# Optimization experiments

Measured on AMD Instinct MI355X. Metric: run time of the kernel, lower is better.

## Reference

```python
import jax, jax.numpy as jnp
import numpy as np

C_S, C_Z, C_H, H, PQ, PV = 384, 128, 16, 12, 4, 8
B, N = 1, 512
W_C = (2.0 / (9.0 * PQ)) ** 0.5
W_L = (1.0 / 3.0) ** 0.5
OUT_IN = H * C_Z + H * C_H + H * PV * 3 + H * PV  # 2112


def setup_inputs() -> dict:
    key = jax.random.key(0)
    ks = jax.random.split(key, 16)
    s_i = jax.random.normal(ks[0], (B, N, C_S), jnp.float32)
    z_ij = jax.random.normal(ks[1], (B, N, N, C_Z), jnp.float32)
    # random rotation matrices via QR
    raw = jax.random.normal(ks[2], (B, N, 3, 3), jnp.float32)
    q, r = jnp.linalg.qr(raw)
    rots = q * jnp.sign(jnp.diagonal(r, axis1=-2, axis2=-1))[..., None, :]
    trans = jax.random.normal(ks[3], (B, N, 3), jnp.float32)
    sc = lambda fan_in: 1.0 / np.sqrt(fan_in)
    Wq = jax.random.normal(ks[4], (C_S, H * C_H), jnp.float32) * sc(C_S)
    Wk = jax.random.normal(ks[5], (C_S, H * C_H), jnp.float32) * sc(C_S)
    Wv = jax.random.normal(ks[6], (C_S, H * C_H), jnp.float32) * sc(C_S)
    Wqp = jax.random.normal(ks[7], (C_S, H * PQ * 3), jnp.float32) * sc(C_S)
    Wkp = jax.random.normal(ks[8], (C_S, H * PQ * 3), jnp.float32) * sc(C_S)
    Wvp = jax.random.normal(ks[9], (C_S, H * PV * 3), jnp.float32) * sc(C_S)
    Wb = jax.random.normal(ks[10], (C_Z, H), jnp.float32) * sc(C_Z)
    gamma = jax.random.normal(ks[11], (1, 1, 1, H), jnp.float32)
    Wout = jax.random.normal(ks[12], (OUT_IN, C_S), jnp.float32) * sc(OUT_IN)
    bout = jnp.zeros((C_S,), jnp.float32)
    return dict(s_i=s_i, z_ij=z_ij, rots=rots, trans=trans, Wq=Wq, Wk=Wk, Wv=Wv,
                Wqp=Wqp, Wkp=Wkp, Wvp=Wvp, Wb=Wb, gamma=gamma, Wout=Wout, bout=bout)


def reference(s_i, z_ij, rots, trans, Wq, Wk, Wv, Wqp, Wkp, Wvp, Wb, gamma, Wout, bout):
    b, n = s_i.shape[0], s_i.shape[1]
    q_h = (s_i @ Wq).reshape(b, n, H, C_H)
    k_h = (s_i @ Wk).reshape(b, n, H, C_H)
    v_h = (s_i @ Wv).reshape(b, n, H, C_H)
    q_hp = (s_i @ Wqp).reshape(b, n, H, PQ, 3)
    k_hp = (s_i @ Wkp).reshape(b, n, H, PQ, 3)
    v_hp = (s_i @ Wvp).reshape(b, n, H, PV, 3)
    b_ij = z_ij @ Wb  # (b,i,j,h)

    t = trans[:, :, None, None, :]  # (b,i,1,1,3)
    apply = lambda x: jnp.einsum('bixy,bihpy->bihpx', rots, x) + t
    inv_apply = lambda x: jnp.einsum('bixy,bihpx->bihpy', rots, x - t)

    qg = apply(q_hp)  # (b,i,h,p,3) global frame
    kg = apply(k_hp)
    # pairwise rigid point distance term: (b,i,j,h)
    diff = qg[:, :, None] - kg[:, None]  # (b,i,j,h,p,3)
    dist2 = jnp.sum(diff * diff, axis=(-1, -2))

    a_s = jnp.einsum('bihd,bjhd->bijh', q_h, k_h) / (C_H ** 0.5)
    a_rigid = (W_C / 2.0) * gamma * dist2
    a = jax.nn.softmax(W_L * (a_s + b_ij - a_rigid), axis=-2)  # softmax over j

    o_hat = jnp.einsum('bijh,bijd->bihd', a, z_ij)
    o = jnp.einsum('bijh,bjhd->bihd', a, v_h)
    vg = apply(v_hp)  # (b,j,h,p,3)
    o_hp = inv_apply(jnp.einsum('bijh,bjhpx->bihpx', a, vg))  # (b,i,h,pv,3)
    o_hp_norm = jnp.sqrt(jnp.sum(o_hp * o_hp, axis=-1))  # (b,i,h,pv)

    cat = jnp.concatenate([
        o_hat.reshape(b, n, H * C_Z),
        o.reshape(b, n, H * C_H),
        o_hp.reshape(b, n, H * PV * 3),
        o_hp_norm.reshape(b, n, H * PV),
    ], axis=-1)
    return cat @ Wout + bout
```

## Files before the change

### kernel.cpp

```cpp
#include <hip/hip_runtime.h>
#include <hip/hip_bf16.h>
#include <math.h>

#define NRES 512
#define CS   384
#define CZ   128
#define NH   12
#define PW   1152
#define JB   64
#define NCH  8
#define PSTRIDE32 1040
#define KS   6
#define KAW  352

static constexpr float WL_F      = 0.57735026918962576f;
static constexpr float HALF_WC_F = 0.11785113019775792f;

typedef __attribute__((ext_vector_type(8))) short short8v;
typedef __attribute__((ext_vector_type(4))) float floatx4;

__device__ __forceinline__ ushort f2b(float f) {
    union { float f; uint u; } v; v.f = f;
    return (ushort)((v.u + 0x7FFFu + ((v.u >> 16) & 1u)) >> 16);
}
__device__ __forceinline__ float b2f(ushort b) {
    union { uint u; float f; } v; v.u = ((uint)b) << 16; return v.f;
}

__global__ __launch_bounds__(256) void k_prep(
    const float* __restrict__ Wq, const float* __restrict__ Wk,
    const float* __restrict__ Wv, const float* __restrict__ Wqp,
    const float* __restrict__ Wkp, const float* __restrict__ Wvp,
    const float* __restrict__ Wb, const float* __restrict__ Wout,
    float* __restrict__ Wcat, ushort* __restrict__ wbt16,
    ushort* __restrict__ woT)
{
    __shared__ ushort tile[64][72];
    const int bx = blockIdx.x;
    if (bx < 384) {
        const int c = bx;
        for (int col = threadIdx.x; col < PW; col += 256) {
            float v;
            if (col < 192)      v = Wq [(size_t)c * 192 + col];
            else if (col < 384) v = Wk [(size_t)c * 192 + col - 192];
            else if (col < 576) v = Wv [(size_t)c * 192 + col - 384];
            else if (col < 720) v = Wqp[(size_t)c * 144 + col - 576];
            else if (col < 864) v = Wkp[(size_t)c * 144 + col - 720];
            else                v = Wvp[(size_t)c * 288 + col - 864];
            Wcat[(size_t)c * PW + col] = v;
        }
        if (bx == 0) {
            for (int idx = threadIdx.x; idx < 16 * 128; idx += 256) {
                const int h = idx >> 7, cc = idx & 127;
                wbt16[idx] = (h < NH) ? f2b(WL_F * Wb[(size_t)cc * NH + h]) : (ushort)0;
            }
        }
    } else {
        const int t = bx - 384;
        const int k0 = (t % 33) * 64, c0 = (t / 33) * 64;
        for (int idx = threadIdx.x; idx < 4096; idx += 256) {
            const int r = idx >> 6, c = idx & 63;
            tile[r][c] = f2b(Wout[(size_t)(k0 + r) * 384 + c0 + c]);
        }
        __syncthreads();
        for (int idx = threadIdx.x; idx < 4096; idx += 256) {
            const int c = idx >> 6, r = idx & 63;
            woT[(size_t)(c0 + c) * 2112 + k0 + r] = tile[r][c];
        }
    }
}

__global__ __launch_bounds__(256) void k_gemm(
    const float* __restrict__ s, const float* __restrict__ Wcat,
    const float* __restrict__ rots, const float* __restrict__ trans,
    float* __restrict__ P)
{
    const int tid = threadIdx.x;
    const int tx = tid & 15, ty = tid >> 4;
    const int n0 = blockIdx.x * 48;
    const int m0 = blockIdx.y * 32;
    __shared__ float As[32][34];
    __shared__ float Bs[32][50];
    __shared__ float rot_lds[32][12];

    if (n0 >= 576) {
        for (int idx = tid; idx < 32 * 12; idx += 256) {
            int r = idx / 12, q = idx % 12;
            rot_lds[r][q] = (q < 9) ? rots[(size_t)(m0 + r) * 9 + q]
                                    : trans[(size_t)(m0 + r) * 3 + q - 9];
        }
    }

    float acc[2][3];
    #pragma unroll
    for (int u = 0; u < 2; ++u)
        #pragma unroll
        for (int v = 0; v < 3; ++v) acc[u][v] = 0.f;

    for (int k0 = 0; k0 < CS; k0 += 32) {
        __syncthreads();
        #pragma unroll
        for (int l = 0; l < 4; ++l) {
            int idx = tid + l * 256;
            int kk = idx & 31, r = idx >> 5;
            As[kk][r] = s[(size_t)(m0 + r) * CS + k0 + kk];
        }
        #pragma unroll
        for (int l = 0; l < 6; ++l) {
            int idx = tid + l * 256;
            int kk = idx / 48, cc = idx % 48;
            Bs[kk][cc] = Wcat[(size_t)(k0 + kk) * PW + n0 + cc];
        }
        __syncthreads();
        #pragma unroll
        for (int kk = 0; kk < 32; ++kk) {
            const float2 a = *(const float2*)&As[kk][ty * 2];
            const float b0 = Bs[kk][tx * 3], b1 = Bs[kk][tx * 3 + 1], b2 = Bs[kk][tx * 3 + 2];
            acc[0][0] += a.x * b0; acc[0][1] += a.x * b1; acc[0][2] += a.x * b2;
            acc[1][0] += a.y * b0; acc[1][1] += a.y * b1; acc[1][2] += a.y * b2;
        }
    }

    #pragma unroll
    for (int u = 0; u < 2; ++u) {
        float v0 = acc[u][0], v1 = acc[u][1], v2 = acc[u][2];
        if (n0 >= 576) {
            const float* RT = rot_lds[ty * 2 + u];
            const float p0 = v0, p1 = v1, p2 = v2;
            v0 = RT[0] * p0 + RT[1] * p1 + RT[2] * p2 + RT[9];
            v1 = RT[3] * p0 + RT[4] * p1 + RT[5] * p2 + RT[10];
            v2 = RT[6] * p0 + RT[7] * p1 + RT[8] * p2 + RT[11];
        }
        float* dst = P + (size_t)(m0 + ty * 2 + u) * PW + n0 + tx * 3;
        dst[0] = v0; dst[1] = v1; dst[2] = v2;
    }
}

__global__ __launch_bounds__(128) void k_ka(
    const float* __restrict__ P, ushort* __restrict__ Kfull,
    ushort* __restrict__ vp2)
{
    const int j = blockIdx.x;
    const int tid = threadIdx.x;
    __shared__ float njs[NH];
    const float* prow = P + (size_t)j * PW;
    const float* kr  = prow + 192;
    const float* vr  = prow + 384;
    const float* kgr = prow + 720;
    const float* vgr = prow + 864;
    if (tid < NH) {
        float s = 0.f;
        #pragma unroll
        for (int e = 0; e < 12; ++e) { const float v = kgr[tid * 12 + e]; s += v * v; }
        njs[tid] = s;
    }
    __syncthreads();
    ushort* dst = Kfull + (size_t)j * KAW;
    for (int t = tid; t < KAW; t += 128) {
        float v;
        if (t < 192)       v = kr[t];
        else if (t < 336)  v = kgr[t - 192];
        else if (t < 348)  v = njs[t - 336];
        else if (t == 348) v = 1.0f;
        else               v = 0.f;
        dst[t] = f2b(v);
    }
    const int p = j >> 1, par = j & 1;
    for (int c = tid; c < 480; c += 128) {
        const float v = (c < 192) ? vr[c] : vgr[c - 192];
        vp2[((size_t)p * 480 + c) * 2 + par] = f2b(v);
    }
}

__global__ __launch_bounds__(256, 6) void k_flash(
    const float* __restrict__ z, const ushort* __restrict__ wbt16,
    const float* __restrict__ gamma, const float* __restrict__ P,
    const ushort* __restrict__ Kfull, const ushort* __restrict__ vp2,
    uint* __restrict__ part)
{
    const int i   = blockIdx.x;
    const int jc  = blockIdx.y;
    const int j0  = jc * JB;
    const int tid = threadIdx.x;
    const int wid = tid >> 6, lane = tid & 63;

    __shared__ __align__(16) short zbT[128 * JB];
    __shared__ __align__(16) char  uni[10240];
    __shared__ float pm[NH], ps[NH];

    short*  BfT     = (short*)uni;
    float*  ltf     = (float*)uni;
    short*  ltb     = (short*)(uni + 4352);
    float4* halfacc = (float4*)(uni + 6400);

    uint* pb32   = part + ((size_t)i * NCH + jc) * PSTRIDE32;
    ushort* pb16 = (ushort*)pb32;
    float* pbf   = (float*)pb32;

    const int jb = wid * 16 + (lane & 15);
    const int ko = (lane >> 4) * 8;

    short8v af[4];
    {
        const float* za = z + ((size_t)i * NRES + j0 + jb) * CZ + ko;
        #pragma unroll
        for (int m = 0; m < 4; ++m) {
            const float4 f0 = *(const float4*)(za + m * 32);
            const float4 f1 = *(const float4*)(za + m * 32 + 4);
            short8v a;
            a[0] = (short)f2b(f0.x); a[1] = (short)f2b(f0.y);
            a[2] = (short)f2b(f0.z); a[3] = (short)f2b(f0.w);
            a[4] = (short)f2b(f1.x); a[5] = (short)f2b(f1.y);
            a[6] = (short)f2b(f1.z); a[7] = (short)f2b(f1.w);
            af[m] = a;
            #pragma unroll
            for (int e = 0; e < 8; ++e) {
                const int c = ko + m * 32 + e;
                zbT[c * 64 + (((jb >> 3) ^ (c & 7)) * 8) + (jb & 7)] = a[e];
            }
        }
    }
    {
        const float* prow = P + (size_t)i * PW;
        for (int t = tid; t < 12 * 352; t += 256) {
            const int h = t / 352, k = t - h * 352;
            float v = 0.f;
            if (k < 192) {
                if ((k >> 4) == h) v = 0.25f * WL_F * prow[k];
            } else if (k < 336) {
                const int e = k - 192;
                if (e / 12 == h) v = 2.f * HALF_WC_F * WL_F * gamma[h] * prow[576 + e];
            } else if (k < 348) {
                if (k - 336 == h) v = -HALF_WC_F * WL_F * gamma[h];
            } else if (k == 348) {
                float ss = 0.f;
                #pragma unroll
                for (int e = 0; e < 12; ++e) {
                    const float x = prow[576 + h * 12 + e];
                    ss += x * x;
                }
                v = -HALF_WC_F * WL_F * gamma[h] * ss;
            }
            BfT[t] = (short)f2b(v);
        }
    }
    __syncthreads();

    floatx4 lacc = {0.f, 0.f, 0.f, 0.f};
    {
        const int n  = lane & 15;
        const int nb = (n < NH) ? n : 0;
        const ushort* arow = Kfull + (size_t)(j0 + jb) * KAW + ko;
        const short*  brow = &BfT[nb * 352 + ko];
        const ushort* wrow = wbt16 + n * 128 + ko;
        #pragma unroll
        for (int st = 0; st < 11; ++st) {
            const short8v a = *(const short8v*)(arow + st * 32);
            const short8v b = *(const short8v*)(brow + st * 32);
            lacc = __builtin_amdgcn_mfma_f32_16x16x32_bf16(a, b, lacc, 0, 0, 0);
        }
        #pragma unroll
        for (int st = 0; st < 4; ++st) {
            const short8v b = *(const short8v*)(wrow + st * 32);
            lacc = __builtin_amdgcn_mfma_f32_16x16x32_bf16(af[st], b, lacc, 0, 0, 0);
        }
    }
    __syncthreads();
    {
        const int n = lane & 15;
        #pragma unroll
        for (int r = 0; r < 4; ++r)
            ltf[n * 68 + wid * 16 + (lane >> 4) * 4 + r] = lacc[r];
    }
    __syncthreads();

    if (tid < 192) {
        const int h = tid >> 4, s = tid & 15;
        float4 v = *(const float4*)&ltf[h * 68 + s * 4];
        float m = fmaxf(fmaxf(v.x, v.y), fmaxf(v.z, v.w));
        #pragma unroll
        for (int o = 1; o < 16; o <<= 1) m = fmaxf(m, __shfl_xor(m, o));
        float4 e;
        e.x = __expf(v.x - m); e.y = __expf(v.y - m);
        e.z = __expf(v.z - m); e.w = __expf(v.w - m);
        float sum = e.x + e.y + e.z + e.w;
        #pragma unroll
        for (int o = 1; o < 16; o <<= 1) sum += __shfl_xor(sum, o);
        *(float4*)&ltf[h * 68 + s * 4] = e;
        const uint lo = (uint)f2b(e.x) | ((uint)f2b(e.y) << 16);
        const uint hi = (uint)f2b(e.z) | ((uint)f2b(e.w) << 16);
        uint* dst = (uint*)&ltb[h * 64 + (((s >> 1) ^ (h & 7)) * 8) + (s & 1) * 4];
        dst[0] = lo; dst[1] = hi;
        if (s == 0) { pm[h] = m; ps[h] = sum; }
    } else {
        const int tt = tid - 192;
        uint* dst = (uint*)&ltb[(12 + (tt >> 4)) * 64 + (tt & 15) * 4];
        dst[0] = 0u; dst[1] = 0u;
    }
    __syncthreads();

    {
        const int hrow = lane & 15;
        const int u0 = (lane >> 4), u1 = u0 + 4;
        const short8v a0 = *(const short8v*)&ltb[hrow * 64 + ((u0 ^ (hrow & 7)) * 8)];
        const short8v a1 = *(const short8v*)&ltb[hrow * 64 + ((u1 ^ (hrow & 7)) * 8)];
        #pragma unroll
        for (int t = 0; t < 2; ++t) {
            const int d = (wid * 2 + t) * 16 + (lane & 15);
            const short8v b0 = *(const short8v*)&zbT[d * 64 + ((u0 ^ (d & 7)) * 8)];
            const short8v b1 = *(const short8v*)&zbT[d * 64 + ((u1 ^ (d & 7)) * 8)];
            floatx4 acc = {0.f, 0.f, 0.f, 0.f};
            acc = __builtin_amdgcn_mfma_f32_16x16x32_bf16(a0, b0, acc, 0, 0, 0);
            acc = __builtin_amdgcn_mfma_f32_16x16x32_bf16(a1, b1, acc, 0, 0, 0);
            #pragma unroll
            for (int r = 0; r < 4; ++r) {
                const int h = u0 * 4 + r;
                if (h < NH) pb16[h * 128 + d] = f2b(acc[r]);
            }
        }
    }

    {
        if (tid < 240) {
            const int half = tid / 120, col = tid % 120;
            const int h = (col < 48) ? (col >> 2) : ((col - 48) / 6);
            const ushort* vb = vp2 + ((size_t)((j0 >> 1) + half * 16) * 480 + col * 4) * 2;
            const float* er = &ltf[h * 68 + half * 32];
            float ax = 0.f, ay = 0.f, az = 0.f, aw = 0.f;
            #pragma unroll 8
            for (int t = 0; t < 16; ++t) {
                const uint4 raw = *(const uint4*)(vb + (size_t)t * 960);
                const float e0 = er[2 * t], e1 = er[2 * t + 1];
                ax += e0 * b2f((ushort)raw.x) + e1 * b2f((ushort)(raw.x >> 16));
                ay += e0 * b2f((ushort)raw.y) + e1 * b2f((ushort)(raw.y >> 16));
                az += e0 * b2f((ushort)raw.z) + e1 * b2f((ushort)(raw.z >> 16));
                aw += e0 * b2f((ushort)raw.w) + e1 * b2f((ushort)(raw.w >> 16));
            }
            halfacc[tid] = make_float4(ax, ay, az, aw);
        }
        __syncthreads();
        if (tid < 120) {
            const float4 s0 = halfacc[tid], s1 = halfacc[tid + 120];
            const int off16 = (tid < 48) ? 1536 + tid * 4 : 1728 + (tid - 48) * 4;
            uint* dst = (uint*)&pb16[off16];
            dst[0] = (uint)f2b(s0.x + s1.x) | ((uint)f2b(s0.y + s1.y) << 16);
            dst[1] = (uint)f2b(s0.z + s1.z) | ((uint)f2b(s0.w + s1.w) << 16);
        }
        if (tid < NH) { pbf[1008 + tid] = pm[tid]; pbf[1020 + tid] = ps[tid]; }
    }
}

__global__ __launch_bounds__(256) void k_combine(
    const uint* __restrict__ part, const float* __restrict__ rots,
    const float* __restrict__ trans, ushort* __restrict__ cat16)
{
    const int i   = blockIdx.x;
    const int tid = threadIdx.x;
    __shared__ float wgt[NCH][NH];
    __shared__ float ohp[288];

    const uint* base = part + (size_t)i * NCH * PSTRIDE32;
    if (tid < NH) {
        const int h = tid;
        float mm[NCH];
        float M = -1e30f;
        #pragma unroll
        for (int c = 0; c < NCH; ++c) {
            mm[c] = ((const float*)(base + c * PSTRIDE32))[1008 + h];
            M = fmaxf(M, mm[c]);
        }
        float S = 0.f;
        #pragma unroll
        for (int c = 0; c < NCH; ++c) {
            const float w = __expf(mm[c] - M);
            S += w * ((const float*)(base + c * PSTRIDE32))[1020 + h];
            wgt[c][h] = w;
        }
        const float inv = 1.0f / S;
        #pragma unroll
        for (int c = 0; c < NCH; ++c) wgt[c][h] *= inv;
    }
    __syncthreads();

    ushort* crow = cat16 + (size_t)i * 2112;
    uint*   crowu = (uint*)crow;
    for (int idx2 = tid; idx2 < 768; idx2 += 256) {
        const int h = idx2 >> 6;
        float v0 = 0.f, v1 = 0.f;
        #pragma unroll
        for (int c = 0; c < NCH; ++c) {
            const uint u = base[c * PSTRIDE32 + idx2];
            const float w = wgt[c][h];
            v0 += b2f((ushort)u) * w;
            v1 += b2f((ushort)(u >> 16)) * w;
        }
        crowu[idx2] = (uint)f2b(v0) | ((uint)f2b(v1) << 16);
    }
    if (tid < 96) {
        const int h = tid >> 3;
        float v0 = 0.f, v1 = 0.f;
        #pragma unroll
        for (int c = 0; c < NCH; ++c) {
            const uint u = base[c * PSTRIDE32 + 768 + tid];
            const float w = wgt[c][h];
            v0 += b2f((ushort)u) * w;
            v1 += b2f((ushort)(u >> 16)) * w;
        }
        crowu[768 + tid] = (uint)f2b(v0) | ((uint)f2b(v1) << 16);
    }
    if (tid < 144) {
        const int h = tid / 12;
        float v0 = 0.f, v1 = 0.f;
        #pragma unroll
        for (int c = 0; c < NCH; ++c) {
            const uint u = base[c * PSTRIDE32 + 864 + tid];
            const float w = wgt[c][h];
            v0 += b2f((ushort)u) * w;
            v1 += b2f((ushort)(u >> 16)) * w;
        }
        ohp[tid * 2] = v0; ohp[tid * 2 + 1] = v1;
    }
    __syncthreads();

    if (tid < 96) {
        const int h = tid >> 3, p = tid & 7;
        float R[9];
        #pragma unroll
        for (int k = 0; k < 9; ++k) R[k] = rots[(size_t)i * 9 + k];
        const float g0 = ohp[h * 24 + p * 3 + 0] - trans[(size_t)i * 3 + 0];
        const float g1 = ohp[h * 24 + p * 3 + 1] - trans[(size_t)i * 3 + 1];
        const float g2 = ohp[h * 24 + p * 3 + 2] - trans[(size_t)i * 3 + 2];
        const float oy0 = R[0] * g0 + R[3] * g1 + R[6] * g2;
        const float oy1 = R[1] * g0 + R[4] * g1 + R[7] * g2;
        const float oy2 = R[2] * g0 + R[5] * g1 + R[8] * g2;
        crow[1728 + h * 24 + p * 3 + 0] = f2b(oy0);
        crow[1728 + h * 24 + p * 3 + 1] = f2b(oy1);
        crow[1728 + h * 24 + p * 3 + 2] = f2b(oy2);
        crow[2016 + h * 8 + p] = f2b(sqrtf(oy0 * oy0 + oy1 * oy1 + oy2 * oy2));
    }
}

__global__ __launch_bounds__(256) void k_out(
    const ushort* __restrict__ cat16, const ushort* __restrict__ woT,
    float* __restrict__ opart)
{
    const int tid = threadIdx.x;
    const int wid = tid >> 6, lane = tid & 63;
    const int wm = wid >> 1, wn = wid & 1;
    const int i0 = blockIdx.x * 32 + wm * 16;
    const int c0 = blockIdx.y * 32 + wn * 16;
    const int k0 = blockIdx.z * 352;
    const ushort* arow = cat16 + (size_t)(i0 + (lane & 15)) * 2112 + k0 + (lane >> 4) * 8;
    const ushort* brow = woT   + (size_t)(c0 + (lane & 15)) * 2112 + k0 + (lane >> 4) * 8;
    floatx4 acc = {0.f, 0.f, 0.f, 0.f};
    #pragma unroll
    for (int st = 0; st < 11; ++st) {
        const short8v a = *(const short8v*)(arow + st * 32);
        const short8v b = *(const short8v*)(brow + st * 32);
        acc = __builtin_amdgcn_mfma_f32_16x16x32_bf16(a, b, acc, 0, 0, 0);
    }
    float* ob = opart + (size_t)blockIdx.z * 512 * 384;
    #pragma unroll
    for (int r = 0; r < 4; ++r) {
        const int i = i0 + (lane >> 4) * 4 + r;
        ob[(size_t)i * 384 + c0 + (lane & 15)] = acc[r];
    }
}

__global__ __launch_bounds__(256) void k_outred(
    const float* __restrict__ opart, const float* __restrict__ bout,
    float* __restrict__ out)
{
    const int e4 = blockIdx.x * 256 + threadIdx.x;
    const float4* p = (const float4*)opart;
    const float4 b = ((const float4*)bout)[e4 % 96];
    float4 r = b;
    #pragma unroll
    for (int k = 0; k < KS; ++k) {
        const float4 v = p[e4 + k * 49152];
        r.x += v.x; r.y += v.y; r.z += v.z; r.w += v.w;
    }
    ((float4*)out)[e4] = r;
}

extern "C" void kernel_launch(void* const* d_in, const int* in_sizes, int n_in,
                              void* d_out, int out_size, void* d_ws, size_t ws_size,
                              hipStream_t stream)
{
    const float* s_i   = (const float*)d_in[0];
    const float* z_ij  = (const float*)d_in[1];
    const float* rots  = (const float*)d_in[2];
    const float* trans = (const float*)d_in[3];
    const float* Wq    = (const float*)d_in[4];
    const float* Wk    = (const float*)d_in[5];
    const float* Wv    = (const float*)d_in[6];
    const float* Wqp   = (const float*)d_in[7];
    const float* Wkp   = (const float*)d_in[8];
    const float* Wvp   = (const float*)d_in[9];
    const float* Wb    = (const float*)d_in[10];
    const float* gamma = (const float*)d_in[11];
    const float* Wout  = (const float*)d_in[12];
    const float* bout  = (const float*)d_in[13];
    float* ws = (float*)d_ws;
    float*  wcat  = ws;
    float*  P     = ws + 442368;
    uint*   part  = (uint*)(P + 589824);
    float*  opart = (float*)part;
    ushort* cat16 = (ushort*)(part + (size_t)512 * NCH * PSTRIDE32);
    ushort* wbt16 = cat16 + 1081344;
    ushort* kfull = wbt16 + 2048;
    ushort* woT   = kfull + 512 * KAW;
    ushort* vp2   = woT + (size_t)384 * 2112;
    float*  out   = (float*)d_out;

    hipLaunchKernelGGL(k_prep, dim3(582), dim3(256), 0, stream,
                       Wq, Wk, Wv, Wqp, Wkp, Wvp, Wb, Wout, wcat, wbt16, woT);
    hipLaunchKernelGGL(k_gemm, dim3(24, 16), dim3(256), 0, stream,
                       s_i, wcat, rots, trans, P);
    hipLaunchKernelGGL(k_ka, dim3(512), dim3(128), 0, stream,
                       P, kfull, vp2);
    hipLaunchKernelGGL(k_flash, dim3(512, NCH), dim3(256), 0, stream,
                       z_ij, wbt16, gamma, P, kfull, vp2, part);
    hipLaunchKernelGGL(k_combine, dim3(512), dim3(256), 0, stream,
                       part, rots, trans, cat16);
    hipLaunchKernelGGL(k_out, dim3(16, 12, KS), dim3(256), 0, stream,
                       cat16, woT, opart);
    hipLaunchKernelGGL(k_outred, dim3(192), dim3(256), 0, stream,
                       opart, bout, out);
}
```

Before: 124.1 us.

## Read projection weights directly in GEMM, drop Wcat copy, vectorize combine

The projection GEMM now picks the source weight matrix per column tile and reads it directly, so the concatenated Wcat buffer and the prep blocks that built it are no longer needed. The prep kernel shrinks to the Wout transpose plus the Wb conversion and now launches after the GEMM and key kernels. The combine kernel's o_hat accumulation loads and stores 4 words per thread instead of 1. This removes one full copy of the projection weights and a dependency step, at the cost of a per-tile branch to select the weight pointer. The GEMM's column tiles of 48 divide 192, 144 and 288 evenly, so no tile straddles two matrices.

```diff
diff --git a/kernel.cpp b/kernel.cpp
--- a/kernel.cpp
+++ b/kernel.cpp
@@ -28,36 +28,13 @@
 }
 
 __global__ __launch_bounds__(256) void k_prep(
-    const float* __restrict__ Wq, const float* __restrict__ Wk,
-    const float* __restrict__ Wv, const float* __restrict__ Wqp,
-    const float* __restrict__ Wkp, const float* __restrict__ Wvp,
     const float* __restrict__ Wb, const float* __restrict__ Wout,
-    float* __restrict__ Wcat, ushort* __restrict__ wbt16,
-    ushort* __restrict__ woT)
+    ushort* __restrict__ wbt16, ushort* __restrict__ woT)
 {
     __shared__ ushort tile[64][72];
     const int bx = blockIdx.x;
-    if (bx < 384) {
-        const int c = bx;
-        for (int col = threadIdx.x; col < PW; col += 256) {
-            float v;
-            if (col < 192)      v = Wq [(size_t)c * 192 + col];
-            else if (col < 384) v = Wk [(size_t)c * 192 + col - 192];
-            else if (col < 576) v = Wv [(size_t)c * 192 + col - 384];
-            else if (col < 720) v = Wqp[(size_t)c * 144 + col - 576];
-            else if (col < 864) v = Wkp[(size_t)c * 144 + col - 720];
-            else                v = Wvp[(size_t)c * 288 + col - 864];
-            Wcat[(size_t)c * PW + col] = v;
-        }
-        if (bx == 0) {
-            for (int idx = threadIdx.x; idx < 16 * 128; idx += 256) {
-                const int h = idx >> 7, cc = idx & 127;
-                wbt16[idx] = (h < NH) ? f2b(WL_F * Wb[(size_t)cc * NH + h]) : (ushort)0;
-            }
-        }
-    } else {
-        const int t = bx - 384;
-        const int k0 = (t % 33) * 64, c0 = (t / 33) * 64;
+    if (bx < 198) {
+        const int k0 = (bx % 33) * 64, c0 = (bx / 33) * 64;
         for (int idx = threadIdx.x; idx < 4096; idx += 256) {
             const int r = idx >> 6, c = idx & 63;
             tile[r][c] = f2b(Wout[(size_t)(k0 + r) * 384 + c0 + c]);
@@ -67,11 +44,19 @@
             const int c = idx >> 6, r = idx & 63;
             woT[(size_t)(c0 + c) * 2112 + k0 + r] = tile[r][c];
         }
+    } else {
+        for (int idx = threadIdx.x; idx < 16 * 128; idx += 256) {
+            const int h = idx >> 7, cc = idx & 127;
+            wbt16[idx] = (h < NH) ? f2b(WL_F * Wb[(size_t)cc * NH + h]) : (ushort)0;
+        }
     }
 }
 
 __global__ __launch_bounds__(256) void k_gemm(
-    const float* __restrict__ s, const float* __restrict__ Wcat,
+    const float* __restrict__ s,
+    const float* __restrict__ Wq, const float* __restrict__ Wk,
+    const float* __restrict__ Wv, const float* __restrict__ Wqp,
+    const float* __restrict__ Wkp, const float* __restrict__ Wvp,
     const float* __restrict__ rots, const float* __restrict__ trans,
     float* __restrict__ P)
 {
@@ -83,6 +68,15 @@
     __shared__ float Bs[32][50];
     __shared__ float rot_lds[32][12];
 
+    const float* Wsel; int W, base;
+    if (n0 < 192)      { Wsel = Wq;  W = 192; base = 0;   }
+    else if (n0 < 384) { Wsel = Wk;  W = 192; base = 192; }
+    else if (n0 < 576) { Wsel = Wv;  W = 192; base = 384; }
+    else if (n0 < 720) { Wsel = Wqp; W = 144; base = 576; }
+    else if (n0 < 864) { Wsel = Wkp; W = 144; base = 720; }
+    else               { Wsel = Wvp; W = 288; base = 864; }
+    const int nb = n0 - base;
+
     if (n0 >= 576) {
         for (int idx = tid; idx < 32 * 12; idx += 256) {
             int r = idx / 12, q = idx % 12;
@@ -109,7 +103,7 @@
         for (int l = 0; l < 6; ++l) {
             int idx = tid + l * 256;
             int kk = idx / 48, cc = idx % 48;
-            Bs[kk][cc] = Wcat[(size_t)(k0 + kk) * PW + n0 + cc];
+            Bs[kk][cc] = Wsel[(size_t)(k0 + kk) * W + nb + cc];
         }
         __syncthreads();
         #pragma unroll
@@ -384,17 +378,26 @@
 
     ushort* crow = cat16 + (size_t)i * 2112;
     uint*   crowu = (uint*)crow;
-    for (int idx2 = tid; idx2 < 768; idx2 += 256) {
-        const int h = idx2 >> 6;
-        float v0 = 0.f, v1 = 0.f;
+    if (tid < 192) {
+        const int h = tid >> 4;
+        float v[8];
+        #pragma unroll
+        for (int e = 0; e < 8; ++e) v[e] = 0.f;
         #pragma unroll
         for (int c = 0; c < NCH; ++c) {
-            const uint u = base[c * PSTRIDE32 + idx2];
+            const uint4 u = *(const uint4*)&base[c * PSTRIDE32 + tid * 4];
             const float w = wgt[c][h];
-            v0 += b2f((ushort)u) * w;
-            v1 += b2f((ushort)(u >> 16)) * w;
-        }
-        crowu[idx2] = (uint)f2b(v0) | ((uint)f2b(v1) << 16);
+            v[0] += b2f((ushort)u.x) * w; v[1] += b2f((ushort)(u.x >> 16)) * w;
+            v[2] += b2f((ushort)u.y) * w; v[3] += b2f((ushort)(u.y >> 16)) * w;
+            v[4] += b2f((ushort)u.z) * w; v[5] += b2f((ushort)(u.z >> 16)) * w;
+            v[6] += b2f((ushort)u.w) * w; v[7] += b2f((ushort)(u.w >> 16)) * w;
+        }
+        uint4 o;
+        o.x = (uint)f2b(v[0]) | ((uint)f2b(v[1]) << 16);
+        o.y = (uint)f2b(v[2]) | ((uint)f2b(v[3]) << 16);
+        o.z = (uint)f2b(v[4]) | ((uint)f2b(v[5]) << 16);
+        o.w = (uint)f2b(v[6]) | ((uint)f2b(v[7]) << 16);
+        *(uint4*)&crowu[tid * 4] = o;
     }
     if (tid < 96) {
         const int h = tid >> 3;
@@ -502,8 +505,7 @@
     const float* Wout  = (const float*)d_in[12];
     const float* bout  = (const float*)d_in[13];
     float* ws = (float*)d_ws;
-    float*  wcat  = ws;
-    float*  P     = ws + 442368;
+    float*  P     = ws;
     uint*   part  = (uint*)(P + 589824);
     float*  opart = (float*)part;
     ushort* cat16 = (ushort*)(part + (size_t)512 * NCH * PSTRIDE32);
@@ -513,12 +515,12 @@
     ushort* vp2   = woT + (size_t)384 * 2112;
     float*  out   = (float*)d_out;
 
-    hipLaunchKernelGGL(k_prep, dim3(582), dim3(256), 0, stream,
-                       Wq, Wk, Wv, Wqp, Wkp, Wvp, Wb, Wout, wcat, wbt16, woT);
     hipLaunchKernelGGL(k_gemm, dim3(24, 16), dim3(256), 0, stream,
-                       s_i, wcat, rots, trans, P);
+                       s_i, Wq, Wk, Wv, Wqp, Wkp, Wvp, rots, trans, P);
     hipLaunchKernelGGL(k_ka, dim3(512), dim3(128), 0, stream,
                        P, kfull, vp2);
+    hipLaunchKernelGGL(k_prep, dim3(199), dim3(256), 0, stream,
+                       Wb, Wout, wbt16, woT);
     hipLaunchKernelGGL(k_flash, dim3(512, NCH), dim3(256), 0, stream,
                        z_ij, wbt16, gamma, P, kfull, vp2, part);
     hipLaunchKernelGGL(k_combine, dim3(512), dim3(256), 0, stream,
```

After: 120.4 us. 2.9% less time.
